# Kernel optimization log

Measured on AMD Instinct MI355X. Metric: run time of the kernel, lower is better.

The kernel has to match this reference:

```python
import jax, jax.numpy as jnp
import numpy as np

N_G = 50000   # glomeruli nodes
N_C = 100000  # immune cell nodes
D_IN = 128    # raw input feature dim
D = 64        # hidden_dim
E_GG = 800000
E_CG = 1600000
E_CC = 1600000
LN_EPS = 1e-5


def _ln(x, s, b):
    m = x.mean(-1, keepdims=True)
    v = ((x - m) ** 2).mean(-1, keepdims=True)
    return (x - m) * jax.lax.rsqrt(v + LN_EPS) * s + b


def _gcn(x, ei, ew, W, b, n):
    # PyG GCNConv: normalize=True, add_self_loops=True (self-loop weight 1)
    xt = x @ W                                   # [n, D]
    row, col = ei[0], ei[1]
    deg = jax.ops.segment_sum(ew, col, num_segments=n) + 1.0  # + self loop
    dinv = jnp.where(deg > 0, jax.lax.rsqrt(deg), 0.0)
    norm = dinv[row] * ew * dinv[col]            # [E]
    out = jax.ops.segment_sum(norm[:, None] * xt[row], col, num_segments=n)
    out = out + (dinv * dinv)[:, None] * xt      # self-loop contribution
    return out + b


def _gin(x_src, x_dst, ei, eps, W, b, n_dst):
    # PyG GINConv (bipartite): nn((1+eps)*x_dst + sum_j x_src[j]), nn = Linear+ReLU
    agg = jax.ops.segment_sum(x_src[ei[0]], ei[1], num_segments=n_dst)
    h = (1.0 + eps) * x_dst + agg
    return jax.nn.relu(h @ W + b)


def setup_inputs() -> dict:
    key = jax.random.key(0)
    ks = jax.random.split(key, 48)
    ctr = [0]
    def nk():
        k = ks[ctr[0]]; ctr[0] += 1; return k
    def w(fan_in, shape):
        return jax.random.normal(nk(), shape, jnp.float32) * (1.0 / np.sqrt(fan_in))
    inp = {}
    inp["x_glom"] = jax.random.normal(nk(), (N_G, D_IN), jnp.float32)
    inp["x_cell"] = jax.random.normal(nk(), (N_C, D_IN), jnp.float32)
    inp["edge_index_gg"] = jax.random.randint(nk(), (2, E_GG), 0, N_G)
    inp["edge_weight_gg"] = jax.random.uniform(nk(), (E_GG,), jnp.float32)
    inp["edge_index_cg"] = jnp.stack([jax.random.randint(nk(), (E_CG,), 0, N_C),
                                      jax.random.randint(nk(), (E_CG,), 0, N_G)])
    inp["edge_index_cc"] = jax.random.randint(nk(), (2, E_CC), 0, N_C)
    # initial per-node-type FC (LazyLinear -> LayerNorm -> ReLU)
    inp["W_in_g"] = w(D_IN, (D_IN, D)); inp["b_in_g"] = jnp.zeros((D,))
    inp["lnig_s"] = jnp.ones((D,));     inp["lnig_b"] = jnp.zeros((D,))
    inp["W_in_c"] = w(D_IN, (D_IN, D)); inp["b_in_c"] = jnp.zeros((D,))
    inp["lnic_s"] = jnp.ones((D,));     inp["lnic_b"] = jnp.zeros((D,))
    for l in ("1", "2"):
        inp["W_gcn" + l] = w(D, (D, D)); inp["b_gcn" + l] = jnp.zeros((D,))
        inp["eps_cg" + l] = jnp.zeros((1,))
        inp["W_cg" + l] = w(D, (D, D)); inp["b_cg" + l] = jnp.zeros((D,))
        inp["eps_cc" + l] = jnp.zeros((1,))
        inp["W_cc" + l] = w(D, (D, D)); inp["b_cc" + l] = jnp.zeros((D,))
        inp["ln" + l + "_s"] = jnp.ones((D,)); inp["ln" + l + "_b"] = jnp.zeros((D,))
    inp["W_out"] = w(D, (D, 3)); inp["b_out"] = jnp.zeros((3,))
    return inp


def reference(x_glom, x_cell, edge_index_gg, edge_weight_gg, edge_index_cg, edge_index_cc,
              W_in_g, b_in_g, lnig_s, lnig_b, W_in_c, b_in_c, lnic_s, lnic_b,
              W_gcn1, b_gcn1, eps_cg1, W_cg1, b_cg1, eps_cc1, W_cc1, b_cc1, ln1_s, ln1_b,
              W_gcn2, b_gcn2, eps_cg2, W_cg2, b_cg2, eps_cc2, W_cc2, b_cc2, ln2_s, ln2_b,
              W_out, b_out):
    # initial per-type FC (dropout identity in eval)
    xg = jax.nn.relu(_ln(x_glom @ W_in_g + b_in_g, lnig_s, lnig_b))
    xc = jax.nn.relu(_ln(x_cell @ W_in_c + b_in_c, lnic_s, lnic_b))
    # hetero MP layer 1: HeteroConv aggr='sum' over relations into each dst type
    g = _gcn(xg, edge_index_gg, edge_weight_gg, W_gcn1, b_gcn1, N_G) \
        + _gin(xc, xg, edge_index_cg, eps_cg1, W_cg1, b_cg1, N_G)
    c = _gin(xc, xc, edge_index_cc, eps_cc1, W_cc1, b_cc1, N_C)
    xg = jax.nn.relu(_ln(g, ln1_s, ln1_b))   # shared LayerNorm across node types
    xc = jax.nn.relu(_ln(c, ln1_s, ln1_b))
    # hetero MP layer 2
    g = _gcn(xg, edge_index_gg, edge_weight_gg, W_gcn2, b_gcn2, N_G) \
        + _gin(xc, xg, edge_index_cg, eps_cg2, W_cg2, b_cg2, N_G)
    c = _gin(xc, xc, edge_index_cc, eps_cc2, W_cc2, b_cc2, N_C)
    xg = jax.nn.relu(_ln(g, ln2_s, ln2_b))
    xc = jax.nn.relu(_ln(c, ln2_s, ln2_b))
    logits = xg @ W_out + b_out
    return jax.nn.softmax(logits, axis=-1)
```

## Files before the change

kernel.cpp:

```cpp
#include <hip/hip_runtime.h>
#include <hip/hip_fp16.h>

#define NG 50000
#define NC 100000
#define DIN 128
#define D 64
#define EGG 800000
#define ECG 1600000
#define ECC 1600000
#define LN_EPS 1e-5f

#define SCAN_N (2 * NG + NC)
#define E_ALL (EGG + ECG + ECC)
#define NBKT 196
#define NBLK 512
#define EPB ((E_ALL + NBLK - 1) / NBLK)

typedef _Float16 f16x8 __attribute__((ext_vector_type(8)));
typedef float f32x4 __attribute__((ext_vector_type(4)));

__device__ __forceinline__ float wave_sum64(float v) {
#pragma unroll
  for (int off = 32; off > 0; off >>= 1) v += __shfl_xor(v, off);
  return v;
}

__device__ __forceinline__ float bcast_lane(float v, int k) {
  return __int_as_float(__builtin_amdgcn_readlane(__float_as_int(v), k));
}

__device__ __forceinline__ float csr_gather_s(
    const int* __restrict__ src, const float* __restrict__ nrm,
    const __half* __restrict__ tab, int e0, int e1, int lane) {
  float a0 = 0.f, a1 = 0.f, a2 = 0.f, a3 = 0.f;
  int e = e0;
  for (; e + 8 <= e1; e += 8) {
    int s0 = src[e + 0], s1 = src[e + 1], s2 = src[e + 2], s3 = src[e + 3];
    int s4 = src[e + 4], s5 = src[e + 5], s6 = src[e + 6], s7 = src[e + 7];
    __half v0 = tab[(size_t)s0 * D + lane];
    __half v1 = tab[(size_t)s1 * D + lane];
    __half v2 = tab[(size_t)s2 * D + lane];
    __half v3 = tab[(size_t)s3 * D + lane];
    __half v4 = tab[(size_t)s4 * D + lane];
    __half v5 = tab[(size_t)s5 * D + lane];
    __half v6 = tab[(size_t)s6 * D + lane];
    __half v7 = tab[(size_t)s7 * D + lane];
    if (nrm) {
      a0 = fmaf(nrm[e + 0], __half2float(v0), a0);
      a1 = fmaf(nrm[e + 1], __half2float(v1), a1);
      a2 = fmaf(nrm[e + 2], __half2float(v2), a2);
      a3 = fmaf(nrm[e + 3], __half2float(v3), a3);
      a0 = fmaf(nrm[e + 4], __half2float(v4), a0);
      a1 = fmaf(nrm[e + 5], __half2float(v5), a1);
      a2 = fmaf(nrm[e + 6], __half2float(v6), a2);
      a3 = fmaf(nrm[e + 7], __half2float(v7), a3);
    } else {
      a0 += __half2float(v0); a1 += __half2float(v1);
      a2 += __half2float(v2); a3 += __half2float(v3);
      a0 += __half2float(v4); a1 += __half2float(v5);
      a2 += __half2float(v6); a3 += __half2float(v7);
    }
  }
  for (; e < e1; ++e) {
    int s = src[e];
    float v = __half2float(tab[(size_t)s * D + lane]);
    if (nrm) a0 = fmaf(nrm[e], v, a0); else a0 += v;
  }
  return (a0 + a1) + (a2 + a3);
}

__global__ __launch_bounds__(256) void fc_in_mfma_kernel(
    const float* __restrict__ x, const float* __restrict__ W,
    const float* __restrict__ b, const float* __restrict__ s,
    const float* __restrict__ beta, __half* __restrict__ y, int n) {
  int wid = (int)(((size_t)blockIdx.x * blockDim.x + threadIdx.x) >> 6);
  int lane = threadIdx.x & 63;
  int r0 = wid * 16;
  if (r0 >= n) return;
  int lo = lane & 15;
  int hi = lane >> 4;

  f16x8 bf[4][4];
#pragma unroll
  for (int kk = 0; kk < 4; ++kk) {
    int kbase = kk * 32 + hi * 8;
#pragma unroll
    for (int t = 0; t < 4; ++t) {
      int c = t * 16 + lo;
      f16x8 v;
#pragma unroll
      for (int j = 0; j < 8; ++j)
        v[j] = (_Float16)W[(kbase + j) * 64 + c];
      bf[kk][t] = v;
    }
  }

  f32x4 acc[4];
#pragma unroll
  for (int t = 0; t < 4; ++t) acc[t] = (f32x4){0.f, 0.f, 0.f, 0.f};

  const float* xr = x + (size_t)(r0 + lo) * DIN;
#pragma unroll
  for (int kk = 0; kk < 4; ++kk) {
    int kbase = kk * 32 + hi * 8;
    float4 xa = *(const float4*)(xr + kbase);
    float4 xb = *(const float4*)(xr + kbase + 4);
    f16x8 af;
    af[0] = (_Float16)xa.x; af[1] = (_Float16)xa.y;
    af[2] = (_Float16)xa.z; af[3] = (_Float16)xa.w;
    af[4] = (_Float16)xb.x; af[5] = (_Float16)xb.y;
    af[6] = (_Float16)xb.z; af[7] = (_Float16)xb.w;
#pragma unroll
    for (int t = 0; t < 4; ++t)
      acc[t] = __builtin_amdgcn_mfma_f32_16x16x32_f16(af, bf[kk][t], acc[t], 0, 0, 0);
  }

  float bc[4], lsv[4], lbv[4];
#pragma unroll
  for (int t = 0; t < 4; ++t) {
    int c = t * 16 + lo;
    bc[t] = b[c]; lsv[t] = s[c]; lbv[t] = beta[c];
  }
#pragma unroll
  for (int reg = 0; reg < 4; ++reg) {
    float v[4];
    float s1 = 0.0f;
#pragma unroll
    for (int t = 0; t < 4; ++t) { v[t] = acc[t][reg] + bc[t]; s1 += v[t]; }
#pragma unroll
    for (int off = 1; off < 16; off <<= 1) s1 += __shfl_xor(s1, off);
    float m = s1 * (1.0f / 64.0f);
    float s2 = 0.0f;
#pragma unroll
    for (int t = 0; t < 4; ++t) { float d = v[t] - m; s2 += d * d; }
#pragma unroll
    for (int off = 1; off < 16; off <<= 1) s2 += __shfl_xor(s2, off);
    float rinv = rsqrtf(s2 * (1.0f / 64.0f) + LN_EPS);
    int r = r0 + hi * 4 + reg;
#pragma unroll
    for (int t = 0; t < 4; ++t) {
      float o = (v[t] - m) * rinv * lsv[t] + lbv[t];
      y[(size_t)r * D + t * 16 + lo] = __float2half(fmaxf(o, 0.0f));
    }
  }
}

__global__ __launch_bounds__(256) void r1_hist_kernel(
    const int* __restrict__ ei_gg, const int* __restrict__ ei_cg,
    const int* __restrict__ ei_cc, int* __restrict__ bhist,
    int* __restrict__ btot) {
  __shared__ int hist[256];
  int t = threadIdx.x;
  int k = blockIdx.x;
  hist[t] = 0;
  __syncthreads();
  int base = k * EPB;
  for (int i = t; i < EPB; i += 256) {
    int e = base + i;
    if (e >= E_ALL) break;
    int key;
    if (e < EGG) key = ei_gg[EGG + e];
    else if (e < EGG + ECG) key = NG + ei_cg[ECG + (e - EGG)];
    else key = 2 * NG + ei_cc[ECC + (e - EGG - ECG)];
    atomicAdd(&hist[key >> 10], 1);
  }
  __syncthreads();
  if (t < NBKT) {
    bhist[t * NBLK + k] = hist[t];
    atomicAdd(&btot[t], hist[t]);
  }
}

__global__ __launch_bounds__(256) void r2b_kernel(
    const int* __restrict__ btot, int* __restrict__ bbase,
    int* __restrict__ S) {
  __shared__ int sh[256];
  int t = threadIdx.x;
  int v = (t < NBKT) ? btot[t] : 0;
  sh[t] = v;
  __syncthreads();
#pragma unroll
  for (int off = 1; off < 256; off <<= 1) {
    int u = (t >= off) ? sh[t - off] : 0;
    __syncthreads();
    sh[t] += u;
    __syncthreads();
  }
  if (t < NBKT) bbase[t] = sh[t] - v;
  if (t == 255) { bbase[NBKT] = sh[255]; S[SCAN_N] = sh[255]; }
}

__global__ __launch_bounds__(512) void r2c_kernel(
    const int* __restrict__ bhist, const int* __restrict__ bbase,
    int* __restrict__ base) {
  int b = blockIdx.x;
  int t = threadIdx.x;
  int lane = t & 63, wv = t >> 6;
  int v = bhist[b * NBLK + t];
  int sc = v;
#pragma unroll
  for (int off = 1; off < 64; off <<= 1) {
    int u = __shfl_up(sc, off);
    if (lane >= off) sc += u;
  }
  __shared__ int ws[8];
  if (lane == 63) ws[wv] = sc;
  __syncthreads();
  int wb = 0;
  for (int i = 0; i < wv; ++i) wb += ws[i];
  base[b * NBLK + t] = bbase[b] + wb + sc - v;
}

__global__ __launch_bounds__(256) void r3_scatter_kernel(
    const int* __restrict__ ei_gg, const float* __restrict__ ew_gg,
    const int* __restrict__ ei_cg, const int* __restrict__ ei_cc,
    const int* __restrict__ base, int* __restrict__ ssort,
    float* __restrict__ wsort) {
  __shared__ int cur[256];
  int t = threadIdx.x;
  int k = blockIdx.x;
  if (t < NBKT) cur[t] = base[t * NBLK + k];
  __syncthreads();
  int bb = k * EPB;
  for (int i = t; i < EPB; i += 256) {
    int e = bb + i;
    if (e >= E_ALL) break;
    int key, s; float w = 0.0f; bool isg = false;
    if (e < EGG) {
      key = ei_gg[EGG + e]; s = ei_gg[e]; w = ew_gg[e]; isg = true;
    } else if (e < EGG + ECG) {
      int q = e - EGG; key = NG + ei_cg[ECG + q]; s = ei_cg[q];
    } else {
      int q = e - EGG - ECG; key = 2 * NG + ei_cc[ECC + q]; s = ei_cc[q];
    }
    int p = atomicAdd(&cur[key >> 10], 1);
    ssort[p] = ((key & 1023) << 17) | s;
    if (isg) wsort[p] = w;
  }
}

__global__ __launch_bounds__(1024) void r4_sort_kernel(
    const int* __restrict__ ssort, const float* __restrict__ wsort,
    const int* __restrict__ bbase, int* __restrict__ S,
    int* __restrict__ srcbuf, float* __restrict__ ewp) {
  int b = blockIdx.x;
  int t = threadIdx.x;
  int e0 = bbase[b], e1 = bbase[b + 1];
  int kbase = b << 10;
  __shared__ int hist[1024];
  __shared__ int sh[1024];
  __shared__ int cur[1024];
  hist[t] = 0;
  __syncthreads();
  for (int e = e0 + t; e < e1; e += 1024)
    atomicAdd(&hist[((unsigned)ssort[e]) >> 17], 1);
  __syncthreads();
  int c = hist[t];
  sh[t] = c;
  __syncthreads();
#pragma unroll
  for (int off = 1; off < 1024; off <<= 1) {
    int u = (t >= off) ? sh[t - off] : 0;
    __syncthreads();
    sh[t] += u;
    __syncthreads();
  }
  int ex = e0 + sh[t] - c;
  int key = kbase + t;
  if (key < SCAN_N) S[key] = ex;
  cur[t] = ex;
  __syncthreads();
  for (int e = e0 + t; e < e1; e += 1024) {
    int rec = ssort[e];
    int lk = ((unsigned)rec) >> 17;
    int p = atomicAdd(&cur[lk], 1);
    srcbuf[p] = rec & 0x1FFFF;
    if (kbase + lk < NG) ewp[p] = wsort[e];
  }
}

__global__ __launch_bounds__(256) void deg_kernel(
    const int* __restrict__ S, const float* __restrict__ ewp,
    float* __restrict__ dinv) {
  int i = (int)(((size_t)blockIdx.x * blockDim.x + threadIdx.x) >> 6);
  int lane = threadIdx.x & 63;
  if (i >= NG) return;
  int e0 = S[i], e1 = S[i + 1];
  float s = 0.0f;
  for (int e = e0 + lane; e < e1; e += 64) s += ewp[e];
  s = wave_sum64(s);
  if (lane == 0) dinv[i] = rsqrtf(s + 1.0f);
}

__global__ __launch_bounds__(256) void nrm_kernel(
    const int* __restrict__ S, const int* __restrict__ srcbuf,
    const float* __restrict__ ewp, const float* __restrict__ dinv,
    float* __restrict__ nrm) {
  int i = (int)(((size_t)blockIdx.x * blockDim.x + threadIdx.x) >> 6);
  int lane = threadIdx.x & 63;
  if (i >= NG) return;
  float di = dinv[i];
  int e0 = S[i], e1 = S[i + 1];
  for (int e = e0 + lane; e < e1; e += 64)
    nrm[e] = dinv[srcbuf[e]] * ewp[e] * di;
}

__global__ __launch_bounds__(256) void glom_layer_kernel(
    const int* __restrict__ rp_gg, const int* __restrict__ rp_cg,
    const int* __restrict__ srcbuf, const float* __restrict__ nrm_gg,
    const __half* __restrict__ xg_old, const __half* __restrict__ xc_old,
    const float* __restrict__ dinv,
    const float* __restrict__ W_gcn, const float* __restrict__ b_gcn,
    const float* __restrict__ eps_cg, const float* __restrict__ W_cg,
    const float* __restrict__ b_cg,
    const float* __restrict__ ls, const float* __restrict__ lb,
    __half* __restrict__ xg_new, int n) {
  int i = (int)(((size_t)blockIdx.x * blockDim.x + threadIdx.x) >> 6);
  int lane = threadIdx.x & 63;
  if (i >= n) return;
  int iu = __builtin_amdgcn_readfirstlane(i);
  int ge0 = __builtin_amdgcn_readfirstlane(rp_gg[iu]);
  int ge1 = __builtin_amdgcn_readfirstlane(rp_gg[iu + 1]);
  int fe0 = __builtin_amdgcn_readfirstlane(rp_cg[iu]);
  int fe1 = __builtin_amdgcn_readfirstlane(rp_cg[iu + 1]);
  float self = __half2float(xg_old[(size_t)iu * D + lane]);
  float di = dinv[iu];
  float accG = di * di * self
             + csr_gather_s(srcbuf, nrm_gg, xg_old, ge0, ge1, lane);
  float accC = csr_gather_s(srcbuf, nullptr, xc_old, fe0, fe1, lane);
  float gcn = b_gcn[lane];
#pragma unroll
  for (int k = 0; k < 64; ++k)
    gcn = fmaf(bcast_lane(accG, k), W_gcn[k * 64 + lane], gcn);
  float h = (1.0f + eps_cg[0]) * self + accC;
  float gin = b_cg[lane];
#pragma unroll
  for (int k = 0; k < 64; ++k)
    gin = fmaf(bcast_lane(h, k), W_cg[k * 64 + lane], gin);
  float g = gcn + fmaxf(gin, 0.0f);
  float m = wave_sum64(g) * (1.0f / 64.0f);
  float d = g - m;
  float var = wave_sum64(d * d) * (1.0f / 64.0f);
  float o = d * rsqrtf(var + LN_EPS) * ls[lane] + lb[lane];
  xg_new[(size_t)iu * D + lane] = __float2half(fmaxf(o, 0.0f));
}

__global__ __launch_bounds__(256) void cell_layer_kernel(
    const int* __restrict__ rp_cc, const int* __restrict__ srcbuf,
    const __half* __restrict__ xc_old,
    const float* __restrict__ eps_cc, const float* __restrict__ W_cc,
    const float* __restrict__ b_cc,
    const float* __restrict__ ls, const float* __restrict__ lb,
    __half* __restrict__ xc_new, int n) {
  int i = (int)(((size_t)blockIdx.x * blockDim.x + threadIdx.x) >> 6);
  int lane = threadIdx.x & 63;
  if (i >= n) return;
  int iu = __builtin_amdgcn_readfirstlane(i);
  int e0 = __builtin_amdgcn_readfirstlane(rp_cc[iu]);
  int e1 = __builtin_amdgcn_readfirstlane(rp_cc[iu + 1]);
  float self = __half2float(xc_old[(size_t)iu * D + lane]);
  float acc = csr_gather_s(srcbuf, nullptr, xc_old, e0, e1, lane);
  float h = (1.0f + eps_cc[0]) * self + acc;
  float gin = b_cc[lane];
#pragma unroll
  for (int k = 0; k < 64; ++k)
    gin = fmaf(bcast_lane(h, k), W_cc[k * 64 + lane], gin);
  float g = fmaxf(gin, 0.0f);
  float m = wave_sum64(g) * (1.0f / 64.0f);
  float d = g - m;
  float var = wave_sum64(d * d) * (1.0f / 64.0f);
  float o = d * rsqrtf(var + LN_EPS) * ls[lane] + lb[lane];
  xc_new[(size_t)iu * D + lane] = __float2half(fmaxf(o, 0.0f));
}

__global__ __launch_bounds__(256) void out_kernel(
    const __half* __restrict__ xg, const float* __restrict__ W,
    const float* __restrict__ b, float* __restrict__ out, int n) {
  int wid = (int)(((size_t)blockIdx.x * blockDim.x + threadIdx.x) >> 6);
  int lane = threadIdx.x & 63;
  if (wid >= n) return;
  float v = __half2float(xg[(size_t)wid * D + lane]);
  float a0 = wave_sum64(v * W[lane * 3 + 0]) + b[0];
  float a1 = wave_sum64(v * W[lane * 3 + 1]) + b[1];
  float a2 = wave_sum64(v * W[lane * 3 + 2]) + b[2];
  float m = fmaxf(a0, fmaxf(a1, a2));
  float e0 = expf(a0 - m), e1 = expf(a1 - m), e2 = expf(a2 - m);
  float inv = 1.0f / (e0 + e1 + e2);
  if (lane == 0) {
    out[(size_t)wid * 3 + 0] = e0 * inv;
    out[(size_t)wid * 3 + 1] = e1 * inv;
    out[(size_t)wid * 3 + 2] = e2 * inv;
  }
}

extern "C" void kernel_launch(void* const* d_in, const int* in_sizes, int n_in,
                              void* d_out, int out_size, void* d_ws, size_t ws_size,
                              hipStream_t stream) {
  const float* x_glom = (const float*)d_in[0];
  const float* x_cell = (const float*)d_in[1];
  const int*   ei_gg  = (const int*)d_in[2];
  const float* ew_gg  = (const float*)d_in[3];
  const int*   ei_cg  = (const int*)d_in[4];
  const int*   ei_cc  = (const int*)d_in[5];
  const float* W_in_g = (const float*)d_in[6];
  const float* b_in_g = (const float*)d_in[7];
  const float* lnig_s = (const float*)d_in[8];
  const float* lnig_b = (const float*)d_in[9];
  const float* W_in_c = (const float*)d_in[10];
  const float* b_in_c = (const float*)d_in[11];
  const float* lnic_s = (const float*)d_in[12];
  const float* lnic_b = (const float*)d_in[13];
  const float* W_outp = (const float*)d_in[34];
  const float* b_outp = (const float*)d_in[35];

  char* P = (char*)d_ws;
  __half* xg0 = (__half*)P;                    P += (size_t)NG * D * 2;
  __half* xg1 = (__half*)P;                    P += (size_t)NG * D * 2;
  __half* xc0 = (__half*)P;                    P += (size_t)NC * D * 2;
  __half* xc1 = (__half*)P;                    P += (size_t)NC * D * 2;
  float* dinv = (float*)P;                     P += (size_t)NG * 4;
  float* nrm  = (float*)P;                     P += (size_t)EGG * 4;
  int* S      = (int*)P;                       P += (size_t)(SCAN_N + 1) * 4;
  int* srcbuf = (int*)P;                       P += (size_t)E_ALL * 4;
  int* bhist  = (int*)P;                       P += (size_t)NBKT * NBLK * 4;
  int* base   = (int*)P;                       P += (size_t)NBKT * NBLK * 4;
  int* btot   = (int*)P;                       P += (size_t)NBKT * 4;
  int* bbase  = (int*)P;                       P += (size_t)(NBKT + 1) * 4;
  int* ssort   = (int*)d_ws;
  float* wsort = (float*)(ssort + E_ALL);
  float* ewp   = wsort + EGG;

  dim3 blk(256);
  auto wgrid = [](long long waves) { return dim3((unsigned)((waves + 3) / 4)); };

  hipMemsetAsync(btot, 0, NBKT * sizeof(int), stream);
  r1_hist_kernel<<<dim3(NBLK), blk, 0, stream>>>(ei_gg, ei_cg, ei_cc, bhist, btot);
  r2b_kernel<<<dim3(1), dim3(256), 0, stream>>>(btot, bbase, S);
  r2c_kernel<<<dim3(NBKT), dim3(512), 0, stream>>>(bhist, bbase, base);
  r3_scatter_kernel<<<dim3(NBLK), blk, 0, stream>>>(
      ei_gg, ew_gg, ei_cg, ei_cc, base, ssort, wsort);
  r4_sort_kernel<<<dim3(NBKT), dim3(1024), 0, stream>>>(
      ssort, wsort, bbase, S, srcbuf, ewp);
  deg_kernel<<<wgrid(NG), blk, 0, stream>>>(S, ewp, dinv);
  nrm_kernel<<<wgrid(NG), blk, 0, stream>>>(S, srcbuf, ewp, dinv, nrm);

  fc_in_mfma_kernel<<<wgrid(NG / 16), blk, 0, stream>>>(
      x_glom, W_in_g, b_in_g, lnig_s, lnig_b, xg0, NG);
  fc_in_mfma_kernel<<<wgrid(NC / 16), blk, 0, stream>>>(
      x_cell, W_in_c, b_in_c, lnic_s, lnic_b, xc0, NC);

  const int* rp_gg = S;
  const int* rp_cg = S + NG;
  const int* rp_cc = S + 2 * NG;
  __half* xg_cur = xg0; __half* xg_nxt = xg1;
  __half* xc_cur = xc0; __half* xc_nxt = xc1;
  for (int l = 0; l < 2; ++l) {
    const float* const* p = (const float* const*)(d_in + 14 + 10 * l);
    const float* W_gcn = p[0]; const float* b_gcn = p[1];
    const float* eps_cg = p[2]; const float* W_cg = p[3]; const float* b_cg = p[4];
    const float* eps_cc = p[5]; const float* W_cc = p[6]; const float* b_cc = p[7];
    const float* ln_s = p[8]; const float* ln_b = p[9];

    glom_layer_kernel<<<wgrid(NG), blk, 0, stream>>>(
        rp_gg, rp_cg, srcbuf, nrm, xg_cur, xc_cur, dinv,
        W_gcn, b_gcn, eps_cg, W_cg, b_cg, ln_s, ln_b, xg_nxt, NG);
    cell_layer_kernel<<<wgrid(NC), blk, 0, stream>>>(
        rp_cc, srcbuf, xc_cur, eps_cc, W_cc, b_cc, ln_s, ln_b, xc_nxt, NC);

    __half* t;
    t = xg_cur; xg_cur = xg_nxt; xg_nxt = t;
    t = xc_cur; xc_cur = xc_nxt; xc_nxt = t;
  }

  out_kernel<<<wgrid(NG), blk, 0, stream>>>(xg_cur, W_outp, b_outp, (float*)d_out, NG);
}
```

Baseline: 503.5 us.

## Gather two neighbor rows per wave using half2 loads and half-wave split

Rewrites the CSR neighbor gather so each half of the wave reads a different edge's feature row as 32 half2 loads, which doubles the edges processed per load instruction. Partial sums from the two halves are combined with a cross-lane shuffle and redistributed back to one feature per lane. The loop runs in chunks of 16 edges and masks the out-of-range edges with a zero weight that still loads row 0. It also reads src and nrm past e1, up to the end of the padded chunk, which wastes work on low-degree nodes and can read past the end of the buffer on the last node.

```diff
diff --git a/kernel.cpp b/kernel.cpp
--- a/kernel.cpp
+++ b/kernel.cpp
@@ -29,44 +29,47 @@
   return __int_as_float(__builtin_amdgcn_readlane(__float_as_int(v), k));
 }
 
-__device__ __forceinline__ float csr_gather_s(
+__device__ __forceinline__ float csr_gather_s2(
     const int* __restrict__ src, const float* __restrict__ nrm,
     const __half* __restrict__ tab, int e0, int e1, int lane) {
-  float a0 = 0.f, a1 = 0.f, a2 = 0.f, a3 = 0.f;
-  int e = e0;
-  for (; e + 8 <= e1; e += 8) {
-    int s0 = src[e + 0], s1 = src[e + 1], s2 = src[e + 2], s3 = src[e + 3];
-    int s4 = src[e + 4], s5 = src[e + 5], s6 = src[e + 6], s7 = src[e + 7];
-    __half v0 = tab[(size_t)s0 * D + lane];
-    __half v1 = tab[(size_t)s1 * D + lane];
-    __half v2 = tab[(size_t)s2 * D + lane];
-    __half v3 = tab[(size_t)s3 * D + lane];
-    __half v4 = tab[(size_t)s4 * D + lane];
-    __half v5 = tab[(size_t)s5 * D + lane];
-    __half v6 = tab[(size_t)s6 * D + lane];
-    __half v7 = tab[(size_t)s7 * D + lane];
-    if (nrm) {
-      a0 = fmaf(nrm[e + 0], __half2float(v0), a0);
-      a1 = fmaf(nrm[e + 1], __half2float(v1), a1);
-      a2 = fmaf(nrm[e + 2], __half2float(v2), a2);
-      a3 = fmaf(nrm[e + 3], __half2float(v3), a3);
-      a0 = fmaf(nrm[e + 4], __half2float(v4), a0);
-      a1 = fmaf(nrm[e + 5], __half2float(v5), a1);
-      a2 = fmaf(nrm[e + 6], __half2float(v6), a2);
-      a3 = fmaf(nrm[e + 7], __half2float(v7), a3);
-    } else {
-      a0 += __half2float(v0); a1 += __half2float(v1);
-      a2 += __half2float(v2); a3 += __half2float(v3);
-      a0 += __half2float(v4); a1 += __half2float(v5);
-      a2 += __half2float(v6); a3 += __half2float(v7);
+  int h = lane >> 5;
+  int m = lane & 31;
+  float ax0 = 0.f, ax1 = 0.f, ax2 = 0.f, ax3 = 0.f;
+  float ay0 = 0.f, ay1 = 0.f, ay2 = 0.f, ay3 = 0.f;
+  for (int e = e0; e < e1; e += 16) {
+#pragma unroll
+    for (int p = 0; p < 8; ++p) {
+      int i0 = e + 2 * p;
+      int se = src[i0];
+      int so = src[i0 + 1];
+      int s = h ? so : se;
+      bool valid = (i0 + h) < e1;
+      float w;
+      if (nrm) {
+        float we = nrm[i0], wo = nrm[i0 + 1];
+        w = h ? wo : we;
+      } else {
+        w = 1.0f;
+      }
+      w = valid ? w : 0.0f;
+      s = valid ? s : 0;
+      __half2 v = *(const __half2*)(tab + (size_t)s * D + 2 * m);
+      float vl = __low2float(v), vh = __high2float(v);
+      switch (p & 3) {
+        case 0: ax0 = fmaf(w, vl, ax0); ay0 = fmaf(w, vh, ay0); break;
+        case 1: ax1 = fmaf(w, vl, ax1); ay1 = fmaf(w, vh, ay1); break;
+        case 2: ax2 = fmaf(w, vl, ax2); ay2 = fmaf(w, vh, ay2); break;
+        default: ax3 = fmaf(w, vl, ax3); ay3 = fmaf(w, vh, ay3); break;
+      }
     }
   }
-  for (; e < e1; ++e) {
-    int s = src[e];
-    float v = __half2float(tab[(size_t)s * D + lane]);
-    if (nrm) a0 = fmaf(nrm[e], v, a0); else a0 += v;
-  }
-  return (a0 + a1) + (a2 + a3);
+  float ax = (ax0 + ax1) + (ax2 + ax3);
+  float ay = (ay0 + ay1) + (ay2 + ay3);
+  ax += __shfl_xor(ax, 32);
+  ay += __shfl_xor(ay, 32);
+  float ev = __shfl(ax, lane >> 1);
+  float od = __shfl(ay, lane >> 1);
+  return (lane & 1) ? od : ev;
 }
 
 __global__ __launch_bounds__(256) void fc_in_mfma_kernel(
@@ -326,8 +329,8 @@
   float self = __half2float(xg_old[(size_t)iu * D + lane]);
   float di = dinv[iu];
   float accG = di * di * self
-             + csr_gather_s(srcbuf, nrm_gg, xg_old, ge0, ge1, lane);
-  float accC = csr_gather_s(srcbuf, nullptr, xc_old, fe0, fe1, lane);
+             + csr_gather_s2(srcbuf, nrm_gg, xg_old, ge0, ge1, lane);
+  float accC = csr_gather_s2(srcbuf, nullptr, xc_old, fe0, fe1, lane);
   float gcn = b_gcn[lane];
 #pragma unroll
   for (int k = 0; k < 64; ++k)
@@ -359,7 +362,7 @@
   int e0 = __builtin_amdgcn_readfirstlane(rp_cc[iu]);
   int e1 = __builtin_amdgcn_readfirstlane(rp_cc[iu + 1]);
   float self = __half2float(xc_old[(size_t)iu * D + lane]);
-  float acc = csr_gather_s(srcbuf, nullptr, xc_old, e0, e1, lane);
+  float acc = csr_gather_s2(srcbuf, nullptr, xc_old, e0, e1, lane);
   float h = (1.0f + eps_cc[0]) * self + acc;
   float gin = b_cc[lane];
 #pragma unroll
```

New measurement: 474.2 us. 5.8% less time.
